# Optimization experiments

Measured on AMD Instinct MI355X. Metric: run time of the kernel, lower is better.

Reference implementation:

```python
import jax, jax.numpy as jnp
import numpy as np

KERNEL_SIZE = 3  # matches init kwarg

def setup_inputs() -> dict:
    key = jax.random.key(0)
    k1, k2, k3, k4 = jax.random.split(key, 4)
    N, C, L, OUT = 32, 64, 2048, 128
    inp = jax.random.normal(k1, (N, C, L), dtype=jnp.float32)
    # adjacency-like dense matrix (tree adjacency may be sparse; dense here)
    m = jax.random.uniform(k2, (N, L, L), dtype=jnp.float32)
    W = jax.random.normal(k3, (OUT, KERNEL_SIZE * C), dtype=jnp.float32) * 0.05
    b = jax.random.normal(k4, (OUT,), dtype=jnp.float32)
    return {"input": inp, "m": m, "W": W, "b": b}

def reference(input, m, W, b):
    # propagate features over the tree adjacency kernel_size-1 times
    ys = [input]
    y = input
    for _ in range(KERNEL_SIZE - 1):
        y = jnp.matmul(y, m)          # (N, C, L) @ (N, L, L) -> (N, C, L)
        ys.append(y)
    cat = jnp.concatenate(ys, axis=1)  # (N, k*C, L)
    # 1x1 conv == channel projection
    out = jnp.einsum('oc,ncl->nol', W, cat) + b[None, :, None]
    return out
```

## Files before the change

### kernel.cpp

```cpp
#include <hip/hip_runtime.h>
#include <hip/hip_bf16.h>

#define NB   32
#define CH   64
#define LL   2048
#define OUTC 128

typedef float  f32x4  __attribute__((ext_vector_type(4)));
typedef short  s16x8  __attribute__((ext_vector_type(8)));
typedef short  s16x4  __attribute__((ext_vector_type(4)));
typedef unsigned short u16;

__device__ __forceinline__ u16 f2bf(float f) {
  unsigned int u = __builtin_bit_cast(unsigned int, f);
  u += 0x7FFFu + ((u >> 16) & 1u);
  return (u16)(u >> 16);
}

__device__ __forceinline__ s16x8 pack8c(const float* v) {
  s16x8 r;
#pragma unroll
  for (int j = 0; j < 8; j += 2) {
    __hip_bfloat162 h = __float22bfloat162_rn(make_float2(v[j], v[j + 1]));
    short2 s;
    __builtin_memcpy(&s, &h, sizeof(s));
    r[j] = s.x; r[j + 1] = s.y;
  }
  return r;
}

__device__ __forceinline__ s16x4 pack4c(const f32x4& v) {
  s16x4 r;
  __hip_bfloat162 h0 = __float22bfloat162_rn(make_float2(v[0], v[1]));
  __hip_bfloat162 h1 = __float22bfloat162_rn(make_float2(v[2], v[3]));
  short2 s0, s1;
  __builtin_memcpy(&s0, &h0, sizeof(s0));
  __builtin_memcpy(&s1, &h1, sizeof(s1));
  r[0] = s0.x; r[1] = s0.y; r[2] = s1.x; r[3] = s1.y;
  return r;
}

#define NX (NB * CH * LL)
#define NW (OUTC * 3 * CH)
__global__ __launch_bounds__(256)
void cvt_inputs(const float* __restrict__ x, const float* __restrict__ W,
                u16* __restrict__ xb, u16* __restrict__ Wb)
{
  const size_t t8 = ((size_t)blockIdx.x * 256 + threadIdx.x) * 8;
  if (t8 < NX) {
    float v[8];
    *(f32x4*)(v)     = *(const f32x4*)(x + t8);
    *(f32x4*)(v + 4) = *(const f32x4*)(x + t8 + 4);
    *(s16x8*)(xb + t8) = pack8c(v);
  } else if (t8 - NX < NW) {
    const size_t w8 = t8 - NX;
    float v[8];
    *(f32x4*)(v)     = *(const f32x4*)(W + w8);
    *(f32x4*)(v + 4) = *(const f32x4*)(W + w8 + 4);
    *(s16x8*)(Wb + w8) = pack8c(v);
  }
}

__global__ __launch_bounds__(256)
void prop1_pack(const u16* __restrict__ xb, const float* __restrict__ m,
                u16* __restrict__ y1, u16* __restrict__ mP)
{
  __shared__ float smem[3][32 * 256];

  const int n    = blockIdx.x >> 3;
  const int lt   = blockIdx.x & 7;
  const int tid  = threadIdx.x;
  const int wave = tid >> 6;
  const int lane = tid & 63;
  const int l15  = lane & 15;
  const int g4   = lane >> 4;
  const int colb = lt * 256 + wave * 64;

  const float* mn   = m + (size_t)n * LL * LL + lt * 256;
  const float* gsrc = mn + (size_t)wave * LL + lane * 4;
  const u16*   ap   = xb + (size_t)n * CH * LL + (size_t)l15 * LL + g4 * 8;
  u16* q0 = mP + (((size_t)n * 64 * LL + colb + l15) * 4 + g4) * 8;
  u16* o  = y1 + (size_t)n * CH * LL + colb + l15;

  f32x4 acc[4][4];
#pragma unroll
  for (int f = 0; f < 4; ++f)
#pragma unroll
    for (int h = 0; h < 4; ++h)
#pragma unroll
      for (int r = 0; r < 4; ++r) acc[f][h][r] = 0.f;

  s16x8 aP[4], aQ[4];

#define ALOAD(R, KB)                                                          \
  { const u16* _ap = ap + (KB) * 32;                                          \
    _Pragma("unroll") for (int f = 0; f < 4; ++f)                             \
      R[f] = *(const s16x8*)(_ap + (size_t)(f * 16) * LL); }

#define GLOAD(BI, KB)                                                         \
  { float* _sb = smem[BI];                                                    \
    _Pragma("unroll") for (int i = 0; i < 8; ++i) {                           \
      const float* _g = gsrc + (size_t)((KB) * 32 + i * 4) * LL;              \
      __builtin_amdgcn_global_load_lds(                                       \
        (const __attribute__((address_space(1))) void*)_g,                    \
        (__attribute__((address_space(3))) void*)(_sb + i * 1024 + wave * 256),\
        16, 0, 0); } }

  ALOAD(aP, 0)
  __builtin_amdgcn_sched_barrier(0);
  GLOAD(0, 0) GLOAD(1, 1)
  __builtin_amdgcn_sched_barrier(0);
  asm volatile("s_waitcnt vmcnt(8)" ::: "memory");
  __builtin_amdgcn_s_barrier();
  __builtin_amdgcn_sched_barrier(0);

#define K1_STEP(KB, CUR, NXT, GI, BI, VN, DOA, DOG, DOBAR)                    \
  {                                                                           \
    if (DOA) {                                                                \
      ALOAD(NXT, (KB) + 1)                                                    \
      __builtin_amdgcn_sched_barrier(0);                                      \
    }                                                                         \
    if (DOG) {                                                                \
      GLOAD(GI, (KB) + 2)                                                     \
      __builtin_amdgcn_sched_barrier(0);                                      \
    }                                                                         \
    const float* _t = smem[BI] + wave * 64 + l15;                             \
    s16x8 _b[4];                                                              \
    _Pragma("unroll") for (int h = 0; h < 4; ++h) {                           \
      float _bv[8];                                                           \
      _Pragma("unroll") for (int j = 0; j < 8; ++j)                           \
        _bv[j] = _t[(g4 * 8 + j) * 256 + h * 16];                             \
      _b[h] = pack8c(_bv);                                                    \
    }                                                                         \
    u16* _q = q0 + (size_t)(KB) * 65536;                                      \
    _Pragma("unroll") for (int h = 0; h < 4; ++h)                             \
      *(s16x8*)(_q + h * 512) = _b[h];                                        \
    _Pragma("unroll") for (int f = 0; f < 4; ++f)                             \
      _Pragma("unroll") for (int h = 0; h < 4; ++h)                           \
        acc[f][h] = __builtin_amdgcn_mfma_f32_16x16x32_bf16(CUR[f], _b[h], acc[f][h], 0, 0, 0); \
    if (DOBAR) {                                                              \
      __builtin_amdgcn_sched_barrier(0);                                      \
      asm volatile("s_waitcnt vmcnt(" VN ")" ::: "memory");                   \
      __builtin_amdgcn_s_barrier();                                           \
      __builtin_amdgcn_sched_barrier(0);                                      \
    }                                                                         \
  }

  K1_STEP(0, aP, aQ, 2, 0, "16", 1, 1, 1)
#pragma unroll 1
  for (int kb = 1; kb <= 55; kb += 6) {
    K1_STEP(kb,     aQ, aP, 0, 1, "20", 1, 1, 1)
    K1_STEP(kb + 1, aP, aQ, 1, 2, "20", 1, 1, 1)
    K1_STEP(kb + 2, aQ, aP, 2, 0, "20", 1, 1, 1)
    K1_STEP(kb + 3, aP, aQ, 0, 1, "20", 1, 1, 1)
    K1_STEP(kb + 4, aQ, aP, 1, 2, "20", 1, 1, 1)
    K1_STEP(kb + 5, aP, aQ, 2, 0, "20", 1, 1, 1)
  }
  K1_STEP(61, aQ, aP, 0, 1, "20", 1, 1, 1)
  K1_STEP(62, aP, aQ, 0, 2, "12", 1, 0, 1)
  K1_STEP(63, aQ, aP, 0, 0, "0",  0, 0, 0)

#pragma unroll
  for (int f = 0; f < 4; ++f)
#pragma unroll
    for (int h = 0; h < 4; ++h)
#pragma unroll
      for (int r = 0; r < 4; ++r) {
        const int row = f * 16 + g4 * 4 + r;
        o[(size_t)row * LL + h * 16] = f2bf(acc[f][h][r]);
      }
}

__global__ __launch_bounds__(256, 3)
void prop2_proj(const u16* __restrict__ y1, const u16* __restrict__ mP,
                const u16* __restrict__ xb, const u16* __restrict__ Wb,
                const float* __restrict__ bias, float* __restrict__ out)
{
  __shared__ u16 yT[128 * 72];

  const int n    = blockIdx.x >> 4;
  const int lt   = blockIdx.x & 15;
  const int tid  = threadIdx.x;
  const int wave = tid >> 6;
  const int lane = tid & 63;
  const int l15  = lane & 15;
  const int g4   = lane >> 4;
  const int colb = lt * 128 + wave * 32;

  const u16* mq = mP + (((size_t)n * 64 * LL + colb + l15) * 4 + g4) * 8;
  const u16* ap = y1 + (size_t)n * CH * LL + (size_t)l15 * LL + g4 * 8;

  f32x4 acc[4][2];
#pragma unroll
  for (int f = 0; f < 4; ++f)
#pragma unroll
    for (int h = 0; h < 2; ++h)
#pragma unroll
      for (int r = 0; r < 4; ++r) acc[f][h][r] = 0.f;

  s16x8 bA0, bA1, bB0, bB1, aA[4], aB[4];

#define K2_LOAD(B0, B1, AV, KB)                                              \
  {                                                                          \
    const u16* _mq = mq + (size_t)(KB) * 65536;                              \
    B0 = *(const s16x8*)(_mq);                                               \
    B1 = *(const s16x8*)(_mq + 512);                                         \
    const u16* _ap = ap + (KB) * 32;                                         \
    _Pragma("unroll") for (int f = 0; f < 4; ++f)                            \
      AV[f] = *(const s16x8*)(_ap + (size_t)(f * 16) * LL);                  \
  }

#define K2_COMP(B0, B1, AV)                                                  \
  _Pragma("unroll") for (int f = 0; f < 4; ++f) {                            \
    acc[f][0] = __builtin_amdgcn_mfma_f32_16x16x32_bf16(AV[f], B0, acc[f][0], 0, 0, 0); \
    acc[f][1] = __builtin_amdgcn_mfma_f32_16x16x32_bf16(AV[f], B1, acc[f][1], 0, 0, 0); \
  }

  K2_LOAD(bA0, bA1, aA, 63)
#pragma unroll 1
  for (int kb = 63; kb >= 1; kb -= 2) {
    K2_LOAD(bB0, bB1, aB, kb - 1)
    K2_COMP(bA0, bA1, aA)
    if (kb - 2 >= 0) K2_LOAD(bA0, bA1, aA, kb - 2)
    K2_COMP(bB0, bB1, aB)
  }

#pragma unroll
  for (int f = 0; f < 4; ++f)
#pragma unroll
    for (int h = 0; h < 2; ++h) {
      const int c = wave * 32 + l15 + 16 * h;
      *(s16x4*)(&yT[c * 72 + f * 16 + g4 * 4]) = pack4c(acc[f][h]);
    }
  __syncthreads();

  f32x4 acc2[8][2];
#pragma unroll
  for (int f = 0; f < 8; ++f)
#pragma unroll
    for (int h = 0; h < 2; ++h)
#pragma unroll
      for (int r = 0; r < 4; ++r) acc2[f][h][r] = 0.f;

  const size_t cb = (size_t)n * CH * LL + colb + l15;
  const u16* xp  = xb + cb + (size_t)(g4 * 8) * LL;
  const u16* y1p = y1 + cb + (size_t)(g4 * 8) * LL;
  const u16* wq  = Wb + (size_t)l15 * 192 + g4 * 8;

#pragma unroll
  for (int kc = 0; kc < 6; ++kc) {
    const int k0 = kc * 32;
    s16x8 b0, b1;
    if (kc < 4) {
      const u16* src = (kc < 2) ? (xp + (size_t)k0 * LL)
                                : (y1p + (size_t)(k0 - 64) * LL);
#pragma unroll
      for (int j = 0; j < 8; ++j) {
        b0[j] = (short)src[(size_t)j * LL];
        b1[j] = (short)src[(size_t)j * LL + 16];
      }
    } else {
      const int rb = (kc - 4) * 32 + g4 * 8;
      b0 = *(const s16x8*)(&yT[(wave * 32 + l15) * 72 + rb]);
      b1 = *(const s16x8*)(&yT[(wave * 32 + l15 + 16) * 72 + rb]);
    }
#pragma unroll
    for (int f = 0; f < 8; ++f) {
      s16x8 af = *(const s16x8*)(wq + (size_t)(f * 16) * 192 + k0);
      acc2[f][0] = __builtin_amdgcn_mfma_f32_16x16x32_bf16(af, b0, acc2[f][0], 0, 0, 0);
      acc2[f][1] = __builtin_amdgcn_mfma_f32_16x16x32_bf16(af, b1, acc2[f][1], 0, 0, 0);
    }
  }

  float* op = out + (size_t)n * OUTC * LL + colb + l15;
#pragma unroll
  for (int f = 0; f < 8; ++f)
#pragma unroll
    for (int r = 0; r < 4; ++r) {
      const int row = f * 16 + g4 * 4 + r;
      op[(size_t)row * LL]      = acc2[f][0][r] + bias[row];
      op[(size_t)row * LL + 16] = acc2[f][1][r] + bias[row];
    }
}

extern "C" void kernel_launch(void* const* d_in, const int* in_sizes, int n_in,
                              void* d_out, int out_size, void* d_ws, size_t ws_size,
                              hipStream_t stream)
{
  const float* x = (const float*)d_in[0];
  const float* m = (const float*)d_in[1];
  const float* W = (const float*)d_in[2];
  const float* b = (const float*)d_in[3];
  float* out = (float*)d_out;

  u16* y1 = (u16*)d_ws;
  u16* xb = y1 + (size_t)NB * CH * LL;
  u16* Wb = xb + (size_t)NB * CH * LL;
  u16* mP = (u16*)((char*)d_ws + (25u << 20));

  cvt_inputs<<<dim3(2060), dim3(256), 0, stream>>>(x, W, xb, Wb);
  prop1_pack<<<dim3(NB * 8), dim3(256), 0, stream>>>(xb, m, y1, mP);
  prop2_proj<<<dim3(NB * 16), dim3(256), 0, stream>>>(y1, mP, xb, Wb, b, out);
}
```

Baseline: 262.5 us.

## Stage adjacency tiles through LDS with async triple-buffered global_load_lds pipeline

The second propagation kernel's B-operand (pre-swizzled adjacency) loads now go through a three-slot LDS ring filled by async global_load_lds, with explicit vmcnt waits and barriers, instead of direct global-to-register loads. A-operand loads stay in registers but are double-buffered one step ahead. The intent is deeper prefetching of the large m stream so more memory latency overlaps MFMA work, without extra VGPRs. The cost is a workgroup barrier every k-step, hand-counted waitcnt values and extra LDS use that may lower occupancy.

```diff
diff --git a/kernel.cpp b/kernel.cpp
--- a/kernel.cpp
+++ b/kernel.cpp
@@ -176,6 +176,7 @@
                 const u16* __restrict__ xb, const u16* __restrict__ Wb,
                 const float* __restrict__ bias, float* __restrict__ out)
 {
+  __shared__ u16 smem2[3][4096];
   __shared__ u16 yT[128 * 72];
 
   const int n    = blockIdx.x >> 4;
@@ -187,7 +188,8 @@
   const int g4   = lane >> 4;
   const int colb = lt * 128 + wave * 32;
 
-  const u16* mq = mP + (((size_t)n * 64 * LL + colb + l15) * 4 + g4) * 8;
+  const u16* gsrc2 = mP + ((size_t)n * 64 * LL + lt * 128) * 32
+                        + wave * 1024 + lane * 8;
   const u16* ap = y1 + (size_t)n * CH * LL + (size_t)l15 * LL + g4 * 8;
 
   f32x4 acc[4][2];
@@ -198,32 +200,69 @@
 #pragma unroll
       for (int r = 0; r < 4; ++r) acc[f][h][r] = 0.f;
 
-  s16x8 bA0, bA1, bB0, bB1, aA[4], aB[4];
-
-#define K2_LOAD(B0, B1, AV, KB)                                              \
-  {                                                                          \
-    const u16* _mq = mq + (size_t)(KB) * 65536;                              \
-    B0 = *(const s16x8*)(_mq);                                               \
-    B1 = *(const s16x8*)(_mq + 512);                                         \
-    const u16* _ap = ap + (KB) * 32;                                         \
-    _Pragma("unroll") for (int f = 0; f < 4; ++f)                            \
-      AV[f] = *(const s16x8*)(_ap + (size_t)(f * 16) * LL);                  \
-  }
-
-#define K2_COMP(B0, B1, AV)                                                  \
-  _Pragma("unroll") for (int f = 0; f < 4; ++f) {                            \
-    acc[f][0] = __builtin_amdgcn_mfma_f32_16x16x32_bf16(AV[f], B0, acc[f][0], 0, 0, 0); \
-    acc[f][1] = __builtin_amdgcn_mfma_f32_16x16x32_bf16(AV[f], B1, acc[f][1], 0, 0, 0); \
-  }
-
-  K2_LOAD(bA0, bA1, aA, 63)
+  s16x8 aP2[4], aQ2[4];
+
+#define ALOAD2(R, KB)                                                         \
+  { const u16* _ap = ap + (KB) * 32;                                          \
+    _Pragma("unroll") for (int f = 0; f < 4; ++f)                             \
+      R[f] = *(const s16x8*)(_ap + (size_t)(f * 16) * LL); }
+
+#define GLOAD2(BI, KB)                                                        \
+  { u16* _sb = smem2[BI];                                                     \
+    _Pragma("unroll") for (int i = 0; i < 2; ++i) {                           \
+      const u16* _g = gsrc2 + (size_t)(KB) * 65536 + i * 512;                 \
+      __builtin_amdgcn_global_load_lds(                                       \
+        (const __attribute__((address_space(1))) void*)_g,                    \
+        (__attribute__((address_space(3))) void*)(_sb + wave * 1024 + i * 512),\
+        16, 0, 0); } }
+
+  ALOAD2(aP2, 0)
+  __builtin_amdgcn_sched_barrier(0);
+  GLOAD2(0, 0) GLOAD2(1, 1)
+  __builtin_amdgcn_sched_barrier(0);
+  asm volatile("s_waitcnt vmcnt(2)" ::: "memory");
+  __builtin_amdgcn_s_barrier();
+  __builtin_amdgcn_sched_barrier(0);
+
+#define K2_STEP(KB, CUR, NXT, GI, BI, VN, DOA, DOG, DOBAR)                    \
+  {                                                                           \
+    if (DOA) {                                                                \
+      ALOAD2(NXT, (KB) + 1)                                                   \
+      __builtin_amdgcn_sched_barrier(0);                                      \
+    }                                                                         \
+    if (DOG) {                                                                \
+      GLOAD2(GI, (KB) + 2)                                                    \
+      __builtin_amdgcn_sched_barrier(0);                                      \
+    }                                                                         \
+    asm volatile("s_waitcnt vmcnt(" VN ")" ::: "memory");                     \
+    __builtin_amdgcn_sched_barrier(0);                                        \
+    const u16* _t = smem2[BI] + wave * 1024 + l15 * 32 + g4 * 8;              \
+    s16x8 _b0 = *(const s16x8*)(_t);                                          \
+    s16x8 _b1 = *(const s16x8*)(_t + 512);                                    \
+    _Pragma("unroll") for (int f = 0; f < 4; ++f) {                           \
+      acc[f][0] = __builtin_amdgcn_mfma_f32_16x16x32_bf16(CUR[f], _b0, acc[f][0], 0, 0, 0); \
+      acc[f][1] = __builtin_amdgcn_mfma_f32_16x16x32_bf16(CUR[f], _b1, acc[f][1], 0, 0, 0); \
+    }                                                                         \
+    if (DOBAR) {                                                              \
+      __builtin_amdgcn_sched_barrier(0);                                      \
+      __builtin_amdgcn_s_barrier();                                           \
+      __builtin_amdgcn_sched_barrier(0);                                      \
+    }                                                                         \
+  }
+
+  K2_STEP(0, aP2, aQ2, 2, 0, "6", 1, 1, 1)
 #pragma unroll 1
-  for (int kb = 63; kb >= 1; kb -= 2) {
-    K2_LOAD(bB0, bB1, aB, kb - 1)
-    K2_COMP(bA0, bA1, aA)
-    if (kb - 2 >= 0) K2_LOAD(bA0, bA1, aA, kb - 2)
-    K2_COMP(bB0, bB1, aB)
-  }
+  for (int kb = 1; kb <= 55; kb += 6) {
+    K2_STEP(kb,     aQ2, aP2, 0, 1, "6", 1, 1, 1)
+    K2_STEP(kb + 1, aP2, aQ2, 1, 2, "6", 1, 1, 1)
+    K2_STEP(kb + 2, aQ2, aP2, 2, 0, "6", 1, 1, 1)
+    K2_STEP(kb + 3, aP2, aQ2, 0, 1, "6", 1, 1, 1)
+    K2_STEP(kb + 4, aQ2, aP2, 1, 2, "6", 1, 1, 1)
+    K2_STEP(kb + 5, aP2, aQ2, 2, 0, "6", 1, 1, 1)
+  }
+  K2_STEP(61, aQ2, aP2, 0, 1, "6", 1, 1, 1)
+  K2_STEP(62, aP2, aQ2, 0, 2, "6", 1, 0, 1)
+  K2_STEP(63, aQ2, aP2, 0, 0, "0", 0, 0, 0)
 
 #pragma unroll
   for (int f = 0; f < 4; ++f)
```

Result: faster. 245.7 us (-6.4%).

## Drop packed bf16 copy of m; re-read fp32 m in second propagation

Applied to the files above, without the earlier changes.

The first propagation kernel no longer writes a packed bf16 copy of the adjacency matrix. The second propagation kernel now streams the fp32 matrix directly through the same LDS triple-buffered pipeline and converts it on the fly. It is retiled to 256 columns per block so it matches the first kernel's structure. This trades a 256MB write plus a 256MB read for a second 512MB fp32 read, and it halves the grid size of the second kernel.

```diff
diff --git a/kernel.cpp b/kernel.cpp
--- a/kernel.cpp
+++ b/kernel.cpp
@@ -62,8 +62,8 @@
 }
 
 __global__ __launch_bounds__(256)
-void prop1_pack(const u16* __restrict__ xb, const float* __restrict__ m,
-                u16* __restrict__ y1, u16* __restrict__ mP)
+void prop1(const u16* __restrict__ xb, const float* __restrict__ m,
+           u16* __restrict__ y1)
 {
   __shared__ float smem[3][32 * 256];
 
@@ -79,8 +79,7 @@
   const float* mn   = m + (size_t)n * LL * LL + lt * 256;
   const float* gsrc = mn + (size_t)wave * LL + lane * 4;
   const u16*   ap   = xb + (size_t)n * CH * LL + (size_t)l15 * LL + g4 * 8;
-  u16* q0 = mP + (((size_t)n * 64 * LL + colb + l15) * 4 + g4) * 8;
-  u16* o  = y1 + (size_t)n * CH * LL + colb + l15;
+  u16* o = y1 + (size_t)n * CH * LL + colb + l15;
 
   f32x4 acc[4][4];
 #pragma unroll
@@ -132,9 +131,6 @@
         _bv[j] = _t[(g4 * 8 + j) * 256 + h * 16];                             \
       _b[h] = pack8c(_bv);                                                    \
     }                                                                         \
-    u16* _q = q0 + (size_t)(KB) * 65536;                                      \
-    _Pragma("unroll") for (int h = 0; h < 4; ++h)                             \
-      *(s16x8*)(_q + h * 512) = _b[h];                                        \
     _Pragma("unroll") for (int f = 0; f < 4; ++f)                             \
       _Pragma("unroll") for (int h = 0; h < 4; ++h)                           \
         acc[f][h] = __builtin_amdgcn_mfma_f32_16x16x32_bf16(CUR[f], _b[h], acc[f][h], 0, 0, 0); \
@@ -146,18 +142,18 @@
     }                                                                         \
   }
 
-  K1_STEP(0, aP, aQ, 2, 0, "16", 1, 1, 1)
+  K1_STEP(0, aP, aQ, 2, 0, "12", 1, 1, 1)
 #pragma unroll 1
   for (int kb = 1; kb <= 55; kb += 6) {
-    K1_STEP(kb,     aQ, aP, 0, 1, "20", 1, 1, 1)
-    K1_STEP(kb + 1, aP, aQ, 1, 2, "20", 1, 1, 1)
-    K1_STEP(kb + 2, aQ, aP, 2, 0, "20", 1, 1, 1)
-    K1_STEP(kb + 3, aP, aQ, 0, 1, "20", 1, 1, 1)
-    K1_STEP(kb + 4, aQ, aP, 1, 2, "20", 1, 1, 1)
-    K1_STEP(kb + 5, aP, aQ, 2, 0, "20", 1, 1, 1)
-  }
-  K1_STEP(61, aQ, aP, 0, 1, "20", 1, 1, 1)
-  K1_STEP(62, aP, aQ, 0, 2, "12", 1, 0, 1)
+    K1_STEP(kb,     aQ, aP, 0, 1, "12", 1, 1, 1)
+    K1_STEP(kb + 1, aP, aQ, 1, 2, "12", 1, 1, 1)
+    K1_STEP(kb + 2, aQ, aP, 2, 0, "12", 1, 1, 1)
+    K1_STEP(kb + 3, aP, aQ, 0, 1, "12", 1, 1, 1)
+    K1_STEP(kb + 4, aQ, aP, 1, 2, "12", 1, 1, 1)
+    K1_STEP(kb + 5, aP, aQ, 2, 0, "12", 1, 1, 1)
+  }
+  K1_STEP(61, aQ, aP, 0, 1, "12", 1, 1, 1)
+  K1_STEP(62, aP, aQ, 0, 2, "4",  1, 0, 1)
   K1_STEP(63, aQ, aP, 0, 0, "0",  0, 0, 0)
 
 #pragma unroll
@@ -171,74 +167,74 @@
       }
 }
 
-__global__ __launch_bounds__(256, 3)
-void prop2_proj(const u16* __restrict__ y1, const u16* __restrict__ mP,
-                const u16* __restrict__ xb, const u16* __restrict__ Wb,
-                const float* __restrict__ bias, float* __restrict__ out)
+__global__ __launch_bounds__(256)
+void prop2m_proj(const u16* __restrict__ y1, const float* __restrict__ m,
+                 const u16* __restrict__ xb, const u16* __restrict__ Wb,
+                 const float* __restrict__ bias, float* __restrict__ out)
 {
-  __shared__ u16 yT[128 * 72];
-
-  const int n    = blockIdx.x >> 4;
-  const int lt   = blockIdx.x & 15;
+  __shared__ float smem[3][32 * 256];
+
+  const int n    = blockIdx.x >> 3;
+  const int lt   = blockIdx.x & 7;
   const int tid  = threadIdx.x;
   const int wave = tid >> 6;
   const int lane = tid & 63;
   const int l15  = lane & 15;
   const int g4   = lane >> 4;
-  const int colb = lt * 128 + wave * 32;
-
-  const u16* mq = mP + (((size_t)n * 64 * LL + colb + l15) * 4 + g4) * 8;
-  const u16* ap = y1 + (size_t)n * CH * LL + (size_t)l15 * LL + g4 * 8;
-
-  f32x4 acc[4][2];
+  const int colb = lt * 256 + wave * 64;
+
+  const float* mn   = m + (size_t)n * LL * LL + lt * 256;
+  const float* gsrc = mn + (size_t)wave * LL + lane * 4;
+  const u16*   ap   = y1 + (size_t)n * CH * LL + (size_t)l15 * LL + g4 * 8;
+
+  f32x4 acc[4][4];
 #pragma unroll
   for (int f = 0; f < 4; ++f)
 #pragma unroll
-    for (int h = 0; h < 2; ++h)
+    for (int h = 0; h < 4; ++h)
 #pragma unroll
       for (int r = 0; r < 4; ++r) acc[f][h][r] = 0.f;
 
-  s16x8 bA0, bA1, bB0, bB1, aA[4], aB[4];
-
-#define K2_LOAD(B0, B1, AV, KB)                                              \
-  {                                                                          \
-    const u16* _mq = mq + (size_t)(KB) * 65536;                              \
-    B0 = *(const s16x8*)(_mq);                                               \
-    B1 = *(const s16x8*)(_mq + 512);                                         \
-    const u16* _ap = ap + (KB) * 32;                                         \
-    _Pragma("unroll") for (int f = 0; f < 4; ++f)                            \
-      AV[f] = *(const s16x8*)(_ap + (size_t)(f * 16) * LL);                  \
-  }
-
-#define K2_COMP(B0, B1, AV)                                                  \
-  _Pragma("unroll") for (int f = 0; f < 4; ++f) {                            \
-    acc[f][0] = __builtin_amdgcn_mfma_f32_16x16x32_bf16(AV[f], B0, acc[f][0], 0, 0, 0); \
-    acc[f][1] = __builtin_amdgcn_mfma_f32_16x16x32_bf16(AV[f], B1, acc[f][1], 0, 0, 0); \
-  }
-
-  K2_LOAD(bA0, bA1, aA, 63)
+  s16x8 aP[4], aQ[4];
+
+  ALOAD(aP, 0)
+  __builtin_amdgcn_sched_barrier(0);
+  GLOAD(0, 0) GLOAD(1, 1)
+  __builtin_amdgcn_sched_barrier(0);
+  asm volatile("s_waitcnt vmcnt(8)" ::: "memory");
+  __builtin_amdgcn_s_barrier();
+  __builtin_amdgcn_sched_barrier(0);
+
+  K1_STEP(0, aP, aQ, 2, 0, "12", 1, 1, 1)
 #pragma unroll 1
-  for (int kb = 63; kb >= 1; kb -= 2) {
-    K2_LOAD(bB0, bB1, aB, kb - 1)
-    K2_COMP(bA0, bA1, aA)
-    if (kb - 2 >= 0) K2_LOAD(bA0, bA1, aA, kb - 2)
-    K2_COMP(bB0, bB1, aB)
-  }
-
+  for (int kb = 1; kb <= 55; kb += 6) {
+    K1_STEP(kb,     aQ, aP, 0, 1, "12", 1, 1, 1)
+    K1_STEP(kb + 1, aP, aQ, 1, 2, "12", 1, 1, 1)
+    K1_STEP(kb + 2, aQ, aP, 2, 0, "12", 1, 1, 1)
+    K1_STEP(kb + 3, aP, aQ, 0, 1, "12", 1, 1, 1)
+    K1_STEP(kb + 4, aQ, aP, 1, 2, "12", 1, 1, 1)
+    K1_STEP(kb + 5, aP, aQ, 2, 0, "12", 1, 1, 1)
+  }
+  K1_STEP(61, aQ, aP, 0, 1, "12", 1, 1, 1)
+  K1_STEP(62, aP, aQ, 0, 2, "4",  1, 0, 1)
+  K1_STEP(63, aQ, aP, 0, 0, "0",  0, 0, 0)
+
+  __syncthreads();
+  u16* yT = (u16*)&smem[0][0];
 #pragma unroll
   for (int f = 0; f < 4; ++f)
 #pragma unroll
-    for (int h = 0; h < 2; ++h) {
-      const int c = wave * 32 + l15 + 16 * h;
+    for (int h = 0; h < 4; ++h) {
+      const int c = wave * 64 + h * 16 + l15;
       *(s16x4*)(&yT[c * 72 + f * 16 + g4 * 4]) = pack4c(acc[f][h]);
     }
   __syncthreads();
 
-  f32x4 acc2[8][2];
+  f32x4 acc2[8][4];
 #pragma unroll
   for (int f = 0; f < 8; ++f)
 #pragma unroll
-    for (int h = 0; h < 2; ++h)
+    for (int h = 0; h < 4; ++h)
 #pragma unroll
       for (int r = 0; r < 4; ++r) acc2[f][h][r] = 0.f;
 
@@ -250,25 +246,27 @@
 #pragma unroll
   for (int kc = 0; kc < 6; ++kc) {
     const int k0 = kc * 32;
-    s16x8 b0, b1;
+    s16x8 b[4];
     if (kc < 4) {
       const u16* src = (kc < 2) ? (xp + (size_t)k0 * LL)
                                 : (y1p + (size_t)(k0 - 64) * LL);
 #pragma unroll
-      for (int j = 0; j < 8; ++j) {
-        b0[j] = (short)src[(size_t)j * LL];
-        b1[j] = (short)src[(size_t)j * LL + 16];
-      }
+      for (int h = 0; h < 4; ++h)
+#pragma unroll
+        for (int j = 0; j < 8; ++j)
+          b[h][j] = (short)src[(size_t)j * LL + h * 16];
     } else {
       const int rb = (kc - 4) * 32 + g4 * 8;
-      b0 = *(const s16x8*)(&yT[(wave * 32 + l15) * 72 + rb]);
-      b1 = *(const s16x8*)(&yT[(wave * 32 + l15 + 16) * 72 + rb]);
+#pragma unroll
+      for (int h = 0; h < 4; ++h)
+        b[h] = *(const s16x8*)(&yT[(wave * 64 + h * 16 + l15) * 72 + rb]);
     }
 #pragma unroll
     for (int f = 0; f < 8; ++f) {
       s16x8 af = *(const s16x8*)(wq + (size_t)(f * 16) * 192 + k0);
-      acc2[f][0] = __builtin_amdgcn_mfma_f32_16x16x32_bf16(af, b0, acc2[f][0], 0, 0, 0);
-      acc2[f][1] = __builtin_amdgcn_mfma_f32_16x16x32_bf16(af, b1, acc2[f][1], 0, 0, 0);
+#pragma unroll
+      for (int h = 0; h < 4; ++h)
+        acc2[f][h] = __builtin_amdgcn_mfma_f32_16x16x32_bf16(af, b[h], acc2[f][h], 0, 0, 0);
     }
   }
 
@@ -276,11 +274,12 @@
 #pragma unroll
   for (int f = 0; f < 8; ++f)
 #pragma unroll
-    for (int r = 0; r < 4; ++r) {
-      const int row = f * 16 + g4 * 4 + r;
-      op[(size_t)row * LL]      = acc2[f][0][r] + bias[row];
-      op[(size_t)row * LL + 16] = acc2[f][1][r] + bias[row];
-    }
+    for (int h = 0; h < 4; ++h)
+#pragma unroll
+      for (int r = 0; r < 4; ++r) {
+        const int row = f * 16 + g4 * 4 + r;
+        op[(size_t)row * LL + h * 16] = acc2[f][h][r] + bias[row];
+      }
 }
 
 extern "C" void kernel_launch(void* const* d_in, const int* in_sizes, int n_in,
@@ -296,9 +295,8 @@
   u16* y1 = (u16*)d_ws;
   u16* xb = y1 + (size_t)NB * CH * LL;
   u16* Wb = xb + (size_t)NB * CH * LL;
-  u16* mP = (u16*)((char*)d_ws + (25u << 20));
 
   cvt_inputs<<<dim3(2060), dim3(256), 0, stream>>>(x, W, xb, Wb);
-  prop1_pack<<<dim3(NB * 8), dim3(256), 0, stream>>>(xb, m, y1, mP);
-  prop2_proj<<<dim3(NB * 16), dim3(256), 0, stream>>>(y1, mP, xb, Wb, b, out);
-}
+  prop1<<<dim3(NB * 8), dim3(256), 0, stream>>>(xb, m, y1);
+  prop2m_proj<<<dim3(NB * 8), dim3(256), 0, stream>>>(y1, m, xb, Wb, b, out);
+}
```

After: 229.0 us. 1.15x faster.
